# Performance work log

Hardware: AMD Instinct MI355X
Metric: run time of the kernel (lower is better)

Reference implementation:

```python
import jax, jax.numpy as jnp
import numpy as np

T_IN = 4096
T_SAVE = 1024
HIDDEN = 512
INPUT = 256
T0, T1 = 0.0, 1.0  # t_span
SCALE = 0.1


def setup_inputs() -> dict:
    key = jax.random.key(0)
    ks = jax.random.split(key, 6)
    return {
        "x0": jax.random.normal(ks[0], (HIDDEN,), jnp.float32),
        "I_seq": jax.random.normal(ks[1], (T_IN, INPUT), jnp.float32),
        "t_save": jnp.linspace(T0, T1, T_SAVE, dtype=jnp.float32),
        "W_tau": SCALE * jax.random.normal(ks[2], (HIDDEN, HIDDEN), jnp.float32),
        "U_tau": SCALE * jax.random.normal(ks[3], (HIDDEN, INPUT), jnp.float32),
        "b_tau": jnp.zeros((HIDDEN,), jnp.float32),
        "tau0": jnp.full((HIDDEN,), 1.0, jnp.float32),
        "W_f": SCALE * jax.random.normal(ks[4], (HIDDEN, HIDDEN), jnp.float32),
        "U_f": SCALE * jax.random.normal(ks[5], (HIDDEN, INPUT), jnp.float32),
        "b_f": jnp.zeros((HIDDEN,), jnp.float32),
    }


def reference(x0, I_seq, t_save, W_tau, U_tau, b_tau, tau0, W_f, U_f, b_f):
    T_in = I_seq.shape[0]
    t_grid = jnp.linspace(T0, T1, T_in, dtype=x0.dtype)  # input sample times

    def dyn(t, x):
        # zero-order-hold input lookup: searchsorted + clamp (matches torch)
        idx = jnp.clip(jnp.searchsorted(t_grid, t), 0, T_in - 1)
        I = I_seq[idx]
        tau = tau0 + jax.nn.softplus(W_tau @ x + U_tau @ I + b_tau)
        f = jnp.tanh(W_f @ x + U_f @ I + b_f)
        return -x / tau + f

    third = 1.0 / 3.0

    def rk4_step(y0, t0, t1):
        # torchdiffeq 'rk4' = rk4_alt_step_func (Kutta 3/8 rule)
        dt = t1 - t0
        k1 = dyn(t0, y0)
        k2 = dyn(t0 + dt * third, y0 + dt * k1 * third)
        k3 = dyn(t0 + dt * 2.0 * third, y0 + dt * (k2 - k1 * third))
        k4 = dyn(t1, y0 + dt * (k1 - k2 + k3))
        return y0 + (k1 + 3.0 * (k2 + k3) + k4) * dt * 0.125

    def step(y, ts):
        t0, t1 = ts
        y1 = rk4_step(y, t0, t1)
        return y1, y1

    _, ys = jax.lax.scan(step, x0, (t_save[:-1], t_save[1:]))
    # odeint returns solution evaluated at every t_save, starting with x0
    return jnp.concatenate([x0[None, :], ys], axis=0)  # [T_SAVE, HIDDEN]
```

## Files before the change

### kernel.cpp

```cpp
#include <hip/hip_runtime.h>
#include <math.h>

#define HID    512
#define NIN    256
#define TIN    4096
#define NSTEP  1023
#define NEVAL  (NSTEP*4)
#define NWG    16
#define SLICE  32
#define NTH    1024

__device__ __forceinline__ int zoh_index(float t) {
  const float delta = 1.0f / 4095.0f;
  int lo = 0, hi = TIN;
  while (lo < hi) {
    int mid = (lo + hi) >> 1;
    float g = (float)mid * delta;
    if (g < t) lo = mid + 1; else hi = mid;
  }
  return lo > TIN - 1 ? TIN - 1 : lo;
}

__global__ void __launch_bounds__(256)
gu_kernel(const float* __restrict__ I_seq, const float* __restrict__ t_save,
          const float* __restrict__ U_tau, const float* __restrict__ b_tau,
          const float* __restrict__ U_f,   const float* __restrict__ b_f,
          float* __restrict__ gu)
{
  __shared__ float Ish[NIN];
  const int e = blockIdx.x;
  const int tid = threadIdx.x;
  const int n = e >> 2, s = e & 3;
  const float t0 = t_save[n], t1 = t_save[n + 1];
  const float dt = t1 - t0;
  const float third = 1.0f / 3.0f;
  float t;
  if      (s == 0) t = t0;
  else if (s == 1) t = t0 + dt * third;
  else if (s == 2) t = t0 + (dt * 2.0f) * third;
  else             t = t1;
  const int idx = zoh_index(t);
  Ish[tid] = I_seq[idx * NIN + tid];
  __syncthreads();
  float* go = gu + (size_t)e * 1024;
  #pragma unroll
  for (int m = 0; m < 2; ++m) {
    const float* __restrict__ U = m ? U_f : U_tau;
    const float* __restrict__ b = m ? b_f : b_tau;
    #pragma unroll
    for (int hh = 0; hh < 2; ++hh) {
      const int h = tid + hh * 256;
      const float4* __restrict__ Ur = (const float4*)(U + (size_t)h * NIN);
      float acc = 0.f;
      #pragma unroll 8
      for (int k = 0; k < NIN / 4; ++k) {
        float4 u = Ur[k];
        acc = fmaf(u.x, Ish[4*k+0], acc);
        acc = fmaf(u.y, Ish[4*k+1], acc);
        acc = fmaf(u.z, Ish[4*k+2], acc);
        acc = fmaf(u.w, Ish[4*k+3], acc);
      }
      go[m * 512 + h] = acc + b[h];
    }
  }
}

__global__ void __launch_bounds__(NTH, 1)
ltc_main(const float* __restrict__ x0, const float* __restrict__ t_save,
         const float* __restrict__ W_tau, const float* __restrict__ tau0,
         const float* __restrict__ W_f,
         const float* __restrict__ gu,
         unsigned long long* xtag,
         float* __restrict__ out)
{
  const int wg   = blockIdx.x;
  const int tid  = threadIdx.x;
  const int row  = tid >> 4;
  const int seg  = tid & 15;
  const int base = wg * SLICE;

  const float* wrow = ((row < SLICE)
      ? (W_tau + (size_t)(base + row) * HID)
      : (W_f   + (size_t)(base + row - SLICE) * HID)) + seg * 32;

  float4 w4[8];
  #pragma unroll
  for (int t = 0; t < 8; ++t) w4[t] = ((const float4*)wrow)[t];

  __shared__ float xsp[16 * 36];
  __shared__ float pre[64];

  float y0 = 0.f, k1 = 0.f, k2 = 0.f, k3 = 0.f, curx = 0.f, tz = 0.f;
  if (tid < SLICE) {
    y0   = x0[base + tid];
    curx = y0;
    tz   = tau0[base + tid];
    out[base + tid] = y0;
  }

  for (int n = 0; n < NSTEP; ++n) {
    const float t0 = t_save[n], t1 = t_save[n + 1];
    const float dt = t1 - t0;
    #pragma unroll
    for (int s = 0; s < 4; ++s) {
      const int e = (n << 2) + s;

      float gt = 0.f, gf = 0.f;
      if (tid < SLICE) {
        const float* g = gu + (size_t)e * 1024 + base + tid;
        gt = g[0];
        gf = g[512];
      }

      if (tid < HID) {
        float v;
        if (e == 0) {
          v = x0[tid];
        } else {
          const unsigned long long* src = xtag + (size_t)(e & 1) * HID + tid;
          unsigned long long pk;
          do {
            pk = __hip_atomic_load(src, __ATOMIC_RELAXED, __HIP_MEMORY_SCOPE_AGENT);
          } while ((unsigned)(pk >> 32) != (unsigned)e);
          v = __uint_as_float((unsigned)pk);
        }
        xsp[(tid >> 5) * 36 + (tid & 31)] = v;
      }
      __syncthreads();

      float acc = 0.f;
      #pragma unroll
      for (int t = 0; t < 8; ++t) {
        const float4 xv = *reinterpret_cast<const float4*>(&xsp[seg * 36 + 4 * t]);
        acc = fmaf(w4[t].x, xv.x, acc);
        acc = fmaf(w4[t].y, xv.y, acc);
        acc = fmaf(w4[t].z, xv.z, acc);
        acc = fmaf(w4[t].w, xv.w, acc);
      }
      acc += __shfl_xor(acc, 1);
      acc += __shfl_xor(acc, 2);
      acc += __shfl_xor(acc, 4);
      acc += __shfl_xor(acc, 8);
      if ((tid & 15) == 0) pre[row] = acc;
      __syncthreads();

      if (tid < SLICE) {
        const float zt  = pre[tid] + gt;
        const float zf  = pre[SLICE + tid] + gf;
        const float ez  = __expf(-fabsf(zt));
        const float sp  = fmaxf(zt, 0.f) + __logf(1.f + ez);
        const float tau = tz + sp;
        const float ef  = __expf(-2.f * fabsf(zf));
        const float th  = (1.f - ef) / (1.f + ef);
        const float f   = (zf >= 0.f) ? th : -th;
        const float d   = f - curx / tau;
        float xnew;
        if      (s == 0) { k1 = d; xnew = y0 + dt * k1 * (1.0f/3.0f); }
        else if (s == 1) { k2 = d; xnew = y0 + dt * (k2 - k1 * (1.0f/3.0f)); }
        else if (s == 2) { k3 = d; xnew = y0 + dt * (k1 - k2 + k3); }
        else {
          xnew = y0 + (k1 + 3.0f * (k2 + k3) + d) * dt * 0.125f;
          y0 = xnew;
          out[(size_t)(n + 1) * HID + base + tid] = xnew;
        }
        curx = xnew;
        const unsigned long long pk =
            ((unsigned long long)(unsigned)(e + 1) << 32) | (unsigned long long)__float_as_uint(xnew);
        __hip_atomic_store(xtag + (size_t)((e + 1) & 1) * HID + base + tid, pk,
                           __ATOMIC_RELAXED, __HIP_MEMORY_SCOPE_AGENT);
      }
    }
  }
}

extern "C" void kernel_launch(void* const* d_in, const int* in_sizes, int n_in,
                              void* d_out, int out_size, void* d_ws, size_t ws_size,
                              hipStream_t stream) {
  const float* x0     = (const float*)d_in[0];
  const float* I_seq  = (const float*)d_in[1];
  const float* t_save = (const float*)d_in[2];
  const float* W_tau  = (const float*)d_in[3];
  const float* U_tau  = (const float*)d_in[4];
  const float* b_tau  = (const float*)d_in[5];
  const float* tau0   = (const float*)d_in[6];
  const float* W_f    = (const float*)d_in[7];
  const float* U_f    = (const float*)d_in[8];
  const float* b_f    = (const float*)d_in[9];
  float* out = (float*)d_out;

  char* ws = (char*)d_ws;
  unsigned long long* xtag = (unsigned long long*)(ws + 1024);
  float* gu = (float*)(ws + 16384);

  hipMemsetAsync(xtag, 0, 2 * HID * sizeof(unsigned long long), stream);
  gu_kernel<<<NEVAL, 256, 0, stream>>>(I_seq, t_save, U_tau, b_tau, U_f, b_f, gu);

  void* args[] = { (void*)&x0, (void*)&t_save, (void*)&W_tau, (void*)&tau0, (void*)&W_f,
                   (void*)&gu, (void*)&xtag, (void*)&out };
  hipLaunchCooperativeKernel((const void*)ltc_main, dim3(NWG), dim3(NTH),
                             args, 0, stream);
}
```

Baseline: 6.270 ms.

## Tile input projection over evaluations and drop a barrier from the recurrent step

The input-projection kernel now computes a 64-evaluation by 128-row tile per block. Each U row is loaded once into registers and reused across 32 evaluations, so U is no longer re-read for every evaluation. In the sequential main kernel, the two rows owned by each output lane are placed in adjacent 16-lane groups so tau and f can be combined with a shuffle instead of a shared-memory stage plus a second __syncthreads. The x staging buffer is double-buffered and the precomputed gu values are prefetched one evaluation ahead. This shortens the critical path of each of the ~4000 serial evaluations, at the cost of more registers in the gu kernel.

```diff
diff --git a/kernel.cpp b/kernel.cpp
--- a/kernel.cpp
+++ b/kernel.cpp
@@ -9,6 +9,7 @@
 #define NWG    16
 #define SLICE  32
 #define NTH    1024
+#define ETILE  64
 
 __device__ __forceinline__ int zoh_index(float t) {
   const float delta = 1.0f / 4095.0f;
@@ -22,46 +23,73 @@
 }
 
 __global__ void __launch_bounds__(256)
-gu_kernel(const float* __restrict__ I_seq, const float* __restrict__ t_save,
-          const float* __restrict__ U_tau, const float* __restrict__ b_tau,
-          const float* __restrict__ U_f,   const float* __restrict__ b_f,
-          float* __restrict__ gu)
+gu2_kernel(const float* __restrict__ I_seq, const float* __restrict__ t_save,
+           const float* __restrict__ U_tau, const float* __restrict__ b_tau,
+           const float* __restrict__ U_f,   const float* __restrict__ b_f,
+           float* __restrict__ gu)
 {
-  __shared__ float Ish[NIN];
-  const int e = blockIdx.x;
+  __shared__ float Ild[ETILE][NIN];
+  __shared__ int idxs[ETILE];
   const int tid = threadIdx.x;
-  const int n = e >> 2, s = e & 3;
-  const float t0 = t_save[n], t1 = t_save[n + 1];
-  const float dt = t1 - t0;
-  const float third = 1.0f / 3.0f;
-  float t;
-  if      (s == 0) t = t0;
-  else if (s == 1) t = t0 + dt * third;
-  else if (s == 2) t = t0 + (dt * 2.0f) * third;
-  else             t = t1;
-  const int idx = zoh_index(t);
-  Ish[tid] = I_seq[idx * NIN + tid];
+  const int e0 = blockIdx.x * ETILE;
+  const int rb = blockIdx.y;
+
+  if (tid < ETILE) {
+    const int e = e0 + tid;
+    const int ec = e < NEVAL ? e : (NEVAL - 1);
+    const int n = ec >> 2, s = ec & 3;
+    const float t0 = t_save[n], t1 = t_save[n + 1];
+    const float dt = t1 - t0;
+    const float third = 1.0f / 3.0f;
+    float t;
+    if      (s == 0) t = t0;
+    else if (s == 1) t = t0 + dt * third;
+    else if (s == 2) t = t0 + (dt * 2.0f) * third;
+    else             t = t1;
+    idxs[tid] = zoh_index(t);
+  }
   __syncthreads();
-  float* go = gu + (size_t)e * 1024;
-  #pragma unroll
-  for (int m = 0; m < 2; ++m) {
-    const float* __restrict__ U = m ? U_f : U_tau;
-    const float* __restrict__ b = m ? b_f : b_tau;
+  #pragma unroll
+  for (int q = 0; q < 16; ++q) {
+    const int li = q * 256 + tid;
+    const int ee = li >> 6, c4 = li & 63;
+    ((float4*)&Ild[ee][0])[c4] = ((const float4*)(I_seq + (size_t)idxs[ee] * NIN))[c4];
+  }
+  __syncthreads();
+
+  const int half = tid >> 7;
+  const int row  = rb * 128 + (tid & 127);
+  const float* Urow = (row < HID) ? (U_tau + (size_t)row * NIN)
+                                  : (U_f + (size_t)(row - HID) * NIN);
+  const float bb = (row < HID) ? b_tau[row] : b_f[row - HID];
+
+  float acc[32];
+  #pragma unroll
+  for (int k = 0; k < 32; ++k) acc[k] = 0.f;
+
+  #pragma unroll
+  for (int c = 0; c < 8; ++c) {
+    float4 u[8];
     #pragma unroll
-    for (int hh = 0; hh < 2; ++hh) {
-      const int h = tid + hh * 256;
-      const float4* __restrict__ Ur = (const float4*)(U + (size_t)h * NIN);
-      float acc = 0.f;
-      #pragma unroll 8
-      for (int k = 0; k < NIN / 4; ++k) {
-        float4 u = Ur[k];
-        acc = fmaf(u.x, Ish[4*k+0], acc);
-        acc = fmaf(u.y, Ish[4*k+1], acc);
-        acc = fmaf(u.z, Ish[4*k+2], acc);
-        acc = fmaf(u.w, Ish[4*k+3], acc);
-      }
-      go[m * 512 + h] = acc + b[h];
+    for (int j = 0; j < 8; ++j) u[j] = ((const float4*)Urow)[c * 8 + j];
+    #pragma unroll
+    for (int k = 0; k < 32; ++k) {
+      const int ee = half * 32 + k;
+      const float4* iv = (const float4*)&Ild[ee][c * 32];
+      float a = acc[k];
+      #pragma unroll
+      for (int j = 0; j < 8; ++j) {
+        float4 x = iv[j];
+        a = fmaf(u[j].x, x.x, a); a = fmaf(u[j].y, x.y, a);
+        a = fmaf(u[j].z, x.z, a); a = fmaf(u[j].w, x.w, a);
+      }
+      acc[k] = a;
     }
+  }
+  #pragma unroll
+  for (int k = 0; k < 32; ++k) {
+    const int e = e0 + half * 32 + k;
+    if (e < NEVAL) gu[(size_t)e * 1024 + row] = acc[k] + bb;
   }
 }
 
@@ -70,68 +98,76 @@
          const float* __restrict__ W_tau, const float* __restrict__ tau0,
          const float* __restrict__ W_f,
          const float* __restrict__ gu,
-         unsigned long long* xtag,
+         unsigned long long* xslot,
          float* __restrict__ out)
 {
   const int wg   = blockIdx.x;
   const int tid  = threadIdx.x;
-  const int row  = tid >> 4;
   const int seg  = tid & 15;
+  const int m    = (tid >> 4) & 1;
+  const int r    = ((tid >> 6) << 1) | ((tid >> 5) & 1);
   const int base = wg * SLICE;
-
-  const float* wrow = ((row < SLICE)
-      ? (W_tau + (size_t)(base + row) * HID)
-      : (W_f   + (size_t)(base + row - SLICE) * HID)) + seg * 32;
+  const int row  = base + r;
+
+  const float* wrow = ((m == 0)
+      ? (W_tau + (size_t)row * HID)
+      : (W_f   + (size_t)row * HID)) + seg * 32;
 
   float4 w4[8];
   #pragma unroll
   for (int t = 0; t < 8; ++t) w4[t] = ((const float4*)wrow)[t];
 
-  __shared__ float xsp[16 * 36];
-  __shared__ float pre[64];
+  __shared__ float xsp[2][16][36];
+
+  const bool isP = (m == 0) && (seg == 0);
 
   float y0 = 0.f, k1 = 0.f, k2 = 0.f, k3 = 0.f, curx = 0.f, tz = 0.f;
-  if (tid < SLICE) {
-    y0   = x0[base + tid];
+  if (isP) {
+    y0   = x0[row];
     curx = y0;
-    tz   = tau0[base + tid];
-    out[base + tid] = y0;
+    tz   = tau0[row];
+    out[row] = y0;
+  }
+
+  float gtn = 0.f, gfn = 0.f;
+  if (isP) {
+    gtn = gu[row];
+    gfn = gu[HID + row];
   }
 
   for (int n = 0; n < NSTEP; ++n) {
-    const float t0 = t_save[n], t1 = t_save[n + 1];
-    const float dt = t1 - t0;
+    const float dt = isP ? (t_save[n + 1] - t_save[n]) : 0.f;
     #pragma unroll
     for (int s = 0; s < 4; ++s) {
       const int e = (n << 2) + s;
-
-      float gt = 0.f, gf = 0.f;
-      if (tid < SLICE) {
-        const float* g = gu + (size_t)e * 1024 + base + tid;
-        gt = g[0];
-        gf = g[512];
-      }
 
       if (tid < HID) {
         float v;
         if (e == 0) {
           v = x0[tid];
         } else {
-          const unsigned long long* src = xtag + (size_t)(e & 1) * HID + tid;
+          const unsigned long long* src = xslot + (size_t)(e & 1) * HID + tid;
           unsigned long long pk;
           do {
             pk = __hip_atomic_load(src, __ATOMIC_RELAXED, __HIP_MEMORY_SCOPE_AGENT);
           } while ((unsigned)(pk >> 32) != (unsigned)e);
           v = __uint_as_float((unsigned)pk);
         }
-        xsp[(tid >> 5) * 36 + (tid & 31)] = v;
+        xsp[e & 1][tid >> 5][tid & 31] = v;
       }
       __syncthreads();
 
+      const float gt = gtn, gf = gfn;
+      if (isP && e + 1 < NEVAL) {
+        gtn = gu[(size_t)(e + 1) * 1024 + row];
+        gfn = gu[(size_t)(e + 1) * 1024 + HID + row];
+      }
+
+      const float* xs = &xsp[e & 1][seg][0];
       float acc = 0.f;
       #pragma unroll
       for (int t = 0; t < 8; ++t) {
-        const float4 xv = *reinterpret_cast<const float4*>(&xsp[seg * 36 + 4 * t]);
+        const float4 xv = ((const float4*)xs)[t];
         acc = fmaf(w4[t].x, xv.x, acc);
         acc = fmaf(w4[t].y, xv.y, acc);
         acc = fmaf(w4[t].z, xv.z, acc);
@@ -141,12 +177,11 @@
       acc += __shfl_xor(acc, 2);
       acc += __shfl_xor(acc, 4);
       acc += __shfl_xor(acc, 8);
-      if ((tid & 15) == 0) pre[row] = acc;
-      __syncthreads();
-
-      if (tid < SLICE) {
-        const float zt  = pre[tid] + gt;
-        const float zf  = pre[SLICE + tid] + gf;
+      const float other = __shfl_xor(acc, 16);
+
+      if (isP) {
+        const float zt  = acc + gt;
+        const float zf  = other + gf;
         const float ez  = __expf(-fabsf(zt));
         const float sp  = fmaxf(zt, 0.f) + __logf(1.f + ez);
         const float tau = tz + sp;
@@ -161,12 +196,13 @@
         else {
           xnew = y0 + (k1 + 3.0f * (k2 + k3) + d) * dt * 0.125f;
           y0 = xnew;
-          out[(size_t)(n + 1) * HID + base + tid] = xnew;
+          out[(size_t)(n + 1) * HID + row] = xnew;
         }
         curx = xnew;
         const unsigned long long pk =
-            ((unsigned long long)(unsigned)(e + 1) << 32) | (unsigned long long)__float_as_uint(xnew);
-        __hip_atomic_store(xtag + (size_t)((e + 1) & 1) * HID + base + tid, pk,
+            ((unsigned long long)(unsigned)(e + 1) << 32) |
+            (unsigned long long)__float_as_uint(xnew);
+        __hip_atomic_store(xslot + (size_t)((e + 1) & 1) * HID + row, pk,
                            __ATOMIC_RELAXED, __HIP_MEMORY_SCOPE_AGENT);
       }
     }
@@ -189,14 +225,14 @@
   float* out = (float*)d_out;
 
   char* ws = (char*)d_ws;
-  unsigned long long* xtag = (unsigned long long*)(ws + 1024);
+  unsigned long long* xslot = (unsigned long long*)(ws + 1024);
   float* gu = (float*)(ws + 16384);
 
-  hipMemsetAsync(xtag, 0, 2 * HID * sizeof(unsigned long long), stream);
-  gu_kernel<<<NEVAL, 256, 0, stream>>>(I_seq, t_save, U_tau, b_tau, U_f, b_f, gu);
+  hipMemsetAsync(xslot, 0, 2 * HID * sizeof(unsigned long long), stream);
+  gu2_kernel<<<dim3(64, 8), 256, 0, stream>>>(I_seq, t_save, U_tau, b_tau, U_f, b_f, gu);
 
   void* args[] = { (void*)&x0, (void*)&t_save, (void*)&W_tau, (void*)&tau0, (void*)&W_f,
-                   (void*)&gu, (void*)&xtag, (void*)&out };
+                   (void*)&gu, (void*)&xslot, (void*)&out };
   hipLaunchCooperativeKernel((const void*)ltc_main, dim3(NWG), dim3(NTH),
                              args, 0, stream);
 }
```

Measured after the change: 12.37 ms. 1.97x slower.
